# Optimization experiments

Hardware: AMD Instinct MI355X
Metric: run time of the kernel (lower is better)

Reference implementation:

```python
import jax, jax.numpy as jnp
import numpy as np

D_IN = 2048
D_OUT = 2048
NUM_HEADS = 16
HEAD_DIM = D_OUT // NUM_HEADS
LATENT = 256
B, S = 2, 2048


def setup_inputs() -> dict:
    key = jax.random.key(0)
    ks = jax.random.split(key, 7)
    s = lambda fan_in: 1.0 / np.sqrt(fan_in)
    return {
        "x": jax.random.normal(ks[0], (B, S, D_IN), dtype=jnp.float32),
        "W_query": jax.random.normal(ks[1], (D_IN, D_OUT), dtype=jnp.float32) * s(D_IN),
        "W_DKV": jax.random.normal(ks[2], (D_IN, LATENT), dtype=jnp.float32) * s(D_IN),
        "W_UK": jax.random.normal(ks[3], (LATENT, D_OUT), dtype=jnp.float32) * s(LATENT),
        "W_UV": jax.random.normal(ks[4], (LATENT, D_OUT), dtype=jnp.float32) * s(LATENT),
        "W_out": jax.random.normal(ks[5], (D_OUT, D_OUT), dtype=jnp.float32) * s(D_OUT),
        "b_out": jax.random.normal(ks[6], (D_OUT,), dtype=jnp.float32) * 0.01,
    }


def reference(x, W_query, W_DKV, W_UK, W_UV, W_out, b_out):
    b, n, _ = x.shape
    # projections
    q = x @ W_query                      # [b, n, d_out]
    latent = x @ W_DKV                   # [b, n, latent]
    k = latent @ W_UK                    # [b, n, d_out]
    v = latent @ W_UV                    # [b, n, d_out]
    # split heads -> [b, h, n, hd]
    to_heads = lambda t: t.reshape(b, n, NUM_HEADS, HEAD_DIM).transpose(0, 2, 1, 3)
    q, k, v = to_heads(q), to_heads(k), to_heads(v)
    scores = jnp.einsum("bhqd,bhkd->bhqk", q, k)
    # causal mask: q_pos < k_pos masked to -inf (applied BEFORE scaling, as in source)
    qpos = jnp.arange(n)[:, None]
    kpos = jnp.arange(n)[None, :]
    scores = jnp.where(qpos < kpos, -jnp.inf, scores)
    attn = jax.nn.softmax(scores / np.sqrt(HEAD_DIM), axis=-1)
    ctx = jnp.einsum("bhqk,bhkd->bhqd", attn, v)   # [b, h, n, hd]
    ctx = ctx.transpose(0, 2, 1, 3).reshape(b, n, D_OUT)
    return ctx @ W_out + b_out
```

## Files before the change

### kernel.cpp

```cpp
#include <hip/hip_runtime.h>

#define DIN 2048
#define DOUT 2048
#define NHEADS 16
#define HDIM 128
#define LATENT 256
#define BB 2
#define SS 2048
#define MTOT (BB*SS)
#define QLD (DOUT + LATENT)
#define KLD (2*DOUT)

using bf16 = __bf16;
using bf16x8 = __attribute__((ext_vector_type(8))) __bf16;
using f32x4 = __attribute__((ext_vector_type(4))) float;

__device__ __forceinline__ void gload16(const bf16* g, bf16* l) {
    __builtin_amdgcn_global_load_lds(
        (const __attribute__((address_space(1))) void*)g,
        (__attribute__((address_space(3))) void*)l, 16, 0, 0);
}

__global__ void cast_f32_bf16(const float* __restrict__ in, bf16* __restrict__ out, int n) {
    int i = (blockIdx.x * blockDim.x + threadIdx.x) * 8;
    if (i >= n) return;
    float4 a = *(const float4*)(in + i);
    float4 b = *(const float4*)(in + i + 4);
    bf16x8 o;
    o[0] = (bf16)a.x; o[1] = (bf16)a.y; o[2] = (bf16)a.z; o[3] = (bf16)a.w;
    o[4] = (bf16)b.x; o[5] = (bf16)b.y; o[6] = (bf16)b.z; o[7] = (bf16)b.w;
    *(bf16x8*)(out + i) = o;
}

__global__ void transpose_cast(const float* __restrict__ W, bf16* __restrict__ WT, int R, int C) {
    __shared__ float tile[32][33];
    int c0 = blockIdx.x * 32, r0 = blockIdx.y * 32;
    int tx = threadIdx.x & 31, ty = threadIdx.x >> 5;
    #pragma unroll
    for (int i = ty; i < 32; i += 8)
        tile[i][tx] = W[(size_t)(r0 + i) * C + c0 + tx];
    __syncthreads();
    #pragma unroll
    for (int i = ty; i < 32; i += 8)
        WT[(size_t)(c0 + i) * R + r0 + tx] = (bf16)tile[tx][i];
}

__global__ void transpose_v(const bf16* __restrict__ v, bf16* __restrict__ vT) {
    int bh = blockIdx.z;
    int s0 = blockIdx.x * 32, d0 = blockIdx.y * 32;
    __shared__ bf16 t[32][33];
    int tx = threadIdx.x & 31, ty = threadIdx.x >> 5;
    int b = bh >> 4, h = bh & 15;
    #pragma unroll
    for (int i = ty; i < 32; i += 8)
        t[i][tx] = v[(size_t)(b * SS + s0 + i) * KLD + h * HDIM + d0 + tx];
    __syncthreads();
    #pragma unroll
    for (int i = ty; i < 32; i += 8)
        vT[((size_t)bh * HDIM + d0 + i) * SS + s0 + tx] = t[tx][i];
}

template<bool OUT_F32, bool BIAS>
__global__ __launch_bounds__(256) void gemm_bt(const bf16* __restrict__ A,
        const bf16* __restrict__ BT, void* __restrict__ Cp,
        const float* __restrict__ bias, const int Kdim, const int Ald,
        const int Ndim, const int Cld) {
    const int nwg = gridDim.x * gridDim.y;
    int orig = blockIdx.y * gridDim.x + blockIdx.x;
    int swz = (orig & 7) * (nwg >> 3) + (orig >> 3);
    const int n0 = (swz % gridDim.x) * 128, m0 = (swz / gridDim.x) * 128;

    const int tid = threadIdx.x, wave = tid >> 6, lane = tid & 63;
    const int wm = wave >> 1, wn = wave & 1;
    const int lr = lane & 15, lg = lane >> 4;
    __shared__ __align__(16) bf16 As[128][32];
    __shared__ __align__(16) bf16 Bs[128][32];
    f32x4 acc[4][4];
    #pragma unroll
    for (int i = 0; i < 4; ++i)
        #pragma unroll
        for (int j = 0; j < 4; ++j) acc[i][j] = (f32x4){0.f, 0.f, 0.f, 0.f};

    const int sr = lane >> 2;
    const int sc = (lane & 3) * 8;
    const bf16* ga = A  + (size_t)(m0 + wave * 16 + sr) * Ald + sc;
    const bf16* gb = BT + (size_t)(n0 + wave * 16 + sr) * Kdim + sc;
    const size_t strideA64 = (size_t)64 * Ald;
    const size_t strideB64 = (size_t)64 * Kdim;
    bf16* lAd = &As[wave * 16][0];
    bf16* lBd = &Bs[wave * 16][0];

    for (int k0 = 0; k0 < Kdim; k0 += 32) {
        gload16(ga,             lAd);
        gload16(ga + strideA64, lAd + 64 * 32);
        gload16(gb,             lBd);
        gload16(gb + strideB64, lBd + 64 * 32);
        ga += 32; gb += 32;
        __syncthreads();
        bf16x8 af[4], bfr[4];
        #pragma unroll
        for (int i = 0; i < 4; ++i)
            af[i] = *(const bf16x8*)&As[wm * 64 + i * 16 + lr][lg * 8];
        #pragma unroll
        for (int j = 0; j < 4; ++j)
            bfr[j] = *(const bf16x8*)&Bs[wn * 64 + j * 16 + lr][lg * 8];
        #pragma unroll
        for (int i = 0; i < 4; ++i)
            #pragma unroll
            for (int j = 0; j < 4; ++j)
                acc[i][j] = __builtin_amdgcn_mfma_f32_16x16x32_bf16(af[i], bfr[j], acc[i][j], 0, 0, 0);
        __syncthreads();
    }
    #pragma unroll
    for (int i = 0; i < 4; ++i)
        #pragma unroll
        for (int j = 0; j < 4; ++j) {
            const int r0 = m0 + wm * 64 + i * 16 + lg * 4;
            const int c = n0 + wn * 64 + j * 16 + lr;
            #pragma unroll
            for (int r2 = 0; r2 < 4; ++r2) {
                float v = acc[i][j][r2];
                if (BIAS) v += bias[c];
                if (OUT_F32) ((float*)Cp)[(size_t)(r0 + r2) * Cld + c] = v;
                else         ((bf16*)Cp)[(size_t)(r0 + r2) * Cld + c] = (bf16)v;
            }
        }
}

__global__ __launch_bounds__(256) void attn_kernel(const bf16* __restrict__ q,
        const bf16* __restrict__ k, const bf16* __restrict__ vT, bf16* __restrict__ ctx) {
    int orig = blockIdx.y * 16 + blockIdx.x;
    int swz = (orig & 7) * 64 + (orig >> 3);
    const int bx = swz & 15, bh = swz >> 4;
    const int b = bh >> 4, h = bh & 15;
    const int tid = threadIdx.x, wave = tid >> 6, lane = tid & 63;
    const int lr = lane & 15, lg = lane >> 4;

    __shared__ __align__(16) bf16 KsL[64 * 128];
    __shared__ __align__(16) bf16 VsL[128 * 64];
    __shared__ __align__(16) bf16 PsL[64 * 64];

    char* KsB = (char*)KsL; char* VsB = (char*)VsL; char* PsB = (char*)PsL;

    const int krow = tid >> 2, kc0b = (tid & 3) * 64;
    const int vrow = tid >> 1, vc0b = (tid & 1) * 64;
    int kOff[4], vOff[4];
    #pragma unroll
    for (int u = 0; u < 4; ++u) {
        kOff[u] = (krow * 256 + kc0b + u * 16) ^ ((krow & 7) << 4);
        vOff[u] = (vrow * 128 + vc0b + u * 16) ^ ((vrow & 7) << 4);
    }
    const bf16* gkb = k  + ((size_t)b * SS + krow) * KLD + h * HDIM + (tid & 3) * 32;
    const bf16* gvb = vT + ((size_t)bh * HDIM + vrow) * SS + (tid & 1) * 32;

    const float C = 0.12751744f;

    for (int half = 0; half < 2; ++half) {
        const int qt = half ? (31 - bx) : bx;
        const int q0 = qt * 64;

        bf16x8 qf[4];
        const bf16* qbase = q + ((size_t)(b * SS + q0 + wave * 16 + lr)) * QLD + h * HDIM;
        #pragma unroll
        for (int d = 0; d < 4; ++d) qf[d] = *(const bf16x8*)(qbase + d * 32 + lg * 8);

        f32x4 o[8];
        #pragma unroll
        for (int i = 0; i < 8; ++i) o[i] = (f32x4){0.f, 0.f, 0.f, 0.f};
        float m_i[4], l_i[4];
        #pragma unroll
        for (int r = 0; r < 4; ++r) { m_i[r] = -3.0e38f; l_i[r] = 0.f; }

        const int nkt = qt + 1;
        bf16x8 kreg[4], vreg[4];
        #pragma unroll
        for (int u = 0; u < 4; ++u) {
            kreg[u] = *(const bf16x8*)(gkb + (size_t)0 * 64 * KLD + u * 8);
            vreg[u] = *(const bf16x8*)(gvb + 0 * 64 + u * 8);
        }
        #pragma unroll
        for (int u = 0; u < 4; ++u) {
            *(bf16x8*)(KsB + kOff[u]) = kreg[u];
            *(bf16x8*)(VsB + vOff[u]) = vreg[u];
        }
        __syncthreads();

        for (int kt = 0; kt < nkt; ++kt) {
            const int kbase = kt * 64;
            const bool have_next = (kt + 1 < nkt);
            if (have_next) {
                const bf16* gk = gkb + (size_t)(kt + 1) * 64 * KLD;
                const bf16* gv = gvb + (kt + 1) * 64;
                #pragma unroll
                for (int u = 0; u < 4; ++u) {
                    kreg[u] = *(const bf16x8*)(gk + u * 8);
                    vreg[u] = *(const bf16x8*)(gv + u * 8);
                }
            }

            f32x4 sacc[4];
            #pragma unroll
            for (int nf = 0; nf < 4; ++nf) sacc[nf] = (f32x4){0.f, 0.f, 0.f, 0.f};
            __builtin_amdgcn_s_setprio(1);
            #pragma unroll
            for (int nf = 0; nf < 4; ++nf)
                #pragma unroll
                for (int d = 0; d < 4; ++d) {
                    int row = nf * 16 + lr;
                    bf16x8 kf = *(const bf16x8*)(KsB + ((row * 256 + d * 64 + lg * 16) ^ ((row & 7) << 4)));
                    sacc[nf] = __builtin_amdgcn_mfma_f32_16x16x32_bf16(qf[d], kf, sacc[nf], 0, 0, 0);
                }
            __builtin_amdgcn_s_setprio(0);

            float sv[4][4];
            const bool maskt = (kbase + 63 > q0);
            #pragma unroll
            for (int nf = 0; nf < 4; ++nf)
                #pragma unroll
                for (int r = 0; r < 4; ++r) {
                    float s = sacc[nf][r];
                    if (maskt) {
                        int qr = q0 + wave * 16 + lg * 4 + r;
                        int kc = kbase + nf * 16 + lr;
                        if (qr < kc) s = -3.0e38f;
                    }
                    sv[nf][r] = s;
                }
            float corr[4];
            #pragma unroll
            for (int r = 0; r < 4; ++r) {
                float v = fmaxf(fmaxf(sv[0][r], sv[1][r]), fmaxf(sv[2][r], sv[3][r]));
                #pragma unroll
                for (int off = 1; off < 16; off <<= 1) v = fmaxf(v, __shfl_xor(v, off));
                float mnew = fmaxf(m_i[r], v);
                corr[r] = __builtin_amdgcn_exp2f((m_i[r] - mnew) * C);
                m_i[r] = mnew;
            }
            float rsum[4] = {0.f, 0.f, 0.f, 0.f};
            #pragma unroll
            for (int nf = 0; nf < 4; ++nf)
                #pragma unroll
                for (int r = 0; r < 4; ++r) {
                    float p = __builtin_amdgcn_exp2f((sv[nf][r] - m_i[r]) * C);
                    rsum[r] += p;
                    int prow = wave * 16 + lg * 4 + r;
                    *(bf16*)(PsB + ((prow * 128 + (nf * 16 + lr) * 2) ^ ((prow & 7) << 4))) = (bf16)p;
                }
            #pragma unroll
            for (int r = 0; r < 4; ++r) {
                float v = rsum[r];
                #pragma unroll
                for (int off = 1; off < 16; off <<= 1) v += __shfl_xor(v, off);
                l_i[r] = l_i[r] * corr[r] + v;
            }
            #pragma unroll
            for (int df = 0; df < 8; ++df)
                #pragma unroll
                for (int r = 0; r < 4; ++r) o[df][r] *= corr[r];

            __builtin_amdgcn_s_setprio(1);
            #pragma unroll
            for (int ks = 0; ks < 2; ++ks) {
                int prow = wave * 16 + lr;
                bf16x8 pf = *(const bf16x8*)(PsB + ((prow * 128 + ks * 64 + lg * 16) ^ ((prow & 7) << 4)));
                #pragma unroll
                for (int df = 0; df < 8; ++df) {
                    int vr2 = df * 16 + lr;
                    bf16x8 vf = *(const bf16x8*)(VsB + ((vr2 * 128 + ks * 64 + lg * 16) ^ ((vr2 & 7) << 4)));
                    o[df] = __builtin_amdgcn_mfma_f32_16x16x32_bf16(pf, vf, o[df], 0, 0, 0);
                }
            }
            __builtin_amdgcn_s_setprio(0);
            __syncthreads();
            if (have_next) {
                #pragma unroll
                for (int u = 0; u < 4; ++u) {
                    *(bf16x8*)(KsB + kOff[u]) = kreg[u];
                    *(bf16x8*)(VsB + vOff[u]) = vreg[u];
                }
            }
            __syncthreads();
        }

        #pragma unroll
        for (int r = 0; r < 4; ++r) {
            float inv = 1.0f / l_i[r];
            #pragma unroll
            for (int df = 0; df < 8; ++df) {
                int rrow = q0 + wave * 16 + lg * 4 + r;
                int col = h * HDIM + df * 16 + lr;
                ctx[(size_t)(b * SS + rrow) * DOUT + col] = (bf16)(o[df][r] * inv);
            }
        }
    }
}

extern "C" void kernel_launch(void* const* d_in, const int* in_sizes, int n_in,
                              void* d_out, int out_size, void* d_ws, size_t ws_size,
                              hipStream_t stream) {
    const float* x    = (const float*)d_in[0];
    const float* Wq   = (const float*)d_in[1];
    const float* Wdkv = (const float*)d_in[2];
    const float* Wuk  = (const float*)d_in[3];
    const float* Wuv  = (const float*)d_in[4];
    const float* Wout = (const float*)d_in[5];
    const float* bout = (const float*)d_in[6];

    char* ws = (char*)d_ws;
    size_t off = 0;
    auto alloc = [&](size_t bytes) { char* p = ws + off; off = (off + bytes + 255) & ~255ULL; return p; };
    bf16* xb    = (bf16*)alloc((size_t)MTOT * DIN * 2);
    bf16* WqT   = (bf16*)alloc((size_t)DOUT * DIN * 2);
    bf16* WdkvT = (bf16*)alloc((size_t)LATENT * DIN * 2);
    bf16* WukT  = (bf16*)alloc((size_t)DOUT * LATENT * 2);
    bf16* WuvT  = (bf16*)alloc((size_t)DOUT * LATENT * 2);
    bf16* WoutT = (bf16*)alloc((size_t)DOUT * DOUT * 2);
    bf16* qlat  = (bf16*)alloc((size_t)MTOT * QLD * 2);
    bf16* kvb   = (bf16*)alloc((size_t)MTOT * KLD * 2);
    bf16* vT    = (bf16*)alloc((size_t)BB * NHEADS * HDIM * SS * 2);
    bf16* ctx   = (bf16*)alloc((size_t)MTOT * DOUT * 2);

    cast_f32_bf16<<<(MTOT * DIN) / 8 / 256, 256, 0, stream>>>(x, xb, MTOT * DIN);
    transpose_cast<<<dim3(DOUT / 32, DIN / 32), 256, 0, stream>>>(Wq, WqT, DIN, DOUT);
    transpose_cast<<<dim3(LATENT / 32, DIN / 32), 256, 0, stream>>>(Wdkv, WdkvT, DIN, LATENT);
    transpose_cast<<<dim3(DOUT / 32, LATENT / 32), 256, 0, stream>>>(Wuk, WukT, LATENT, DOUT);
    transpose_cast<<<dim3(DOUT / 32, LATENT / 32), 256, 0, stream>>>(Wuv, WuvT, LATENT, DOUT);
    transpose_cast<<<dim3(DOUT / 32, DOUT / 32), 256, 0, stream>>>(Wout, WoutT, DOUT, DOUT);

    gemm_bt<false, false><<<dim3(QLD / 128, MTOT / 128), 256, 0, stream>>>(
        xb, WqT, qlat, nullptr, DIN, DIN, QLD, QLD);
    gemm_bt<false, false><<<dim3(KLD / 128, MTOT / 128), 256, 0, stream>>>(
        qlat + DOUT, WukT, kvb, nullptr, LATENT, QLD, KLD, KLD);

    transpose_v<<<dim3(SS / 32, HDIM / 32, BB * NHEADS), 256, 0, stream>>>(kvb + DOUT, vT);

    attn_kernel<<<dim3(16, BB * NHEADS), 256, 0, stream>>>(qlat, kvb, vT, ctx);

    gemm_bt<true, true><<<dim3(DOUT / 128, MTOT / 128), 256, 0, stream>>>(
        ctx, WoutT, d_out, bout, DOUT, DOUT, DOUT, DOUT);
}
```

Measured before the change: 444.7 us.

## Double-buffer attention K/V tiles with direct global-to-LDS async loads

Replaces the register-staged K/V prefetch in the attention kernel with global_load_lds direct-to-LDS copies into double-buffered shared tiles. This removes one of the two per-iteration barriers and the VGPRs that held the staged tiles. Launch bounds now request 4 blocks per CU. The exchange is double the K/V LDS footprint and a reliance on the async LDS writes being visible after the remaining barrier. The softmax scale constant is also nudged slightly.

```diff
diff --git a/kernel.cpp b/kernel.cpp
--- a/kernel.cpp
+++ b/kernel.cpp
@@ -127,7 +127,7 @@
         }
 }
 
-__global__ __launch_bounds__(256) void attn_kernel(const bf16* __restrict__ q,
+__global__ __launch_bounds__(256, 4) void attn_kernel(const bf16* __restrict__ q,
         const bf16* __restrict__ k, const bf16* __restrict__ vT, bf16* __restrict__ ctx) {
     int orig = blockIdx.y * 16 + blockIdx.x;
     int swz = (orig & 7) * 64 + (orig >> 3);
@@ -136,25 +136,25 @@
     const int tid = threadIdx.x, wave = tid >> 6, lane = tid & 63;
     const int lr = lane & 15, lg = lane >> 4;
 
-    __shared__ __align__(16) bf16 KsL[64 * 128];
-    __shared__ __align__(16) bf16 VsL[128 * 64];
-    __shared__ __align__(16) bf16 PsL[64 * 64];
-
-    char* KsB = (char*)KsL; char* VsB = (char*)VsL; char* PsB = (char*)PsL;
-
-    const int krow = tid >> 2, kc0b = (tid & 3) * 64;
-    const int vrow = tid >> 1, vc0b = (tid & 1) * 64;
-    int kOff[4], vOff[4];
-    #pragma unroll
-    for (int u = 0; u < 4; ++u) {
-        kOff[u] = (krow * 256 + kc0b + u * 16) ^ ((krow & 7) << 4);
-        vOff[u] = (vrow * 128 + vc0b + u * 16) ^ ((vrow & 7) << 4);
+    __shared__ __align__(16) char KsB[2 * 16384];
+    __shared__ __align__(16) char VsB[2 * 16384];
+    __shared__ __align__(16) char PsB[64 * 128];
+
+    int krow[4], kcolE[4];
+    #pragma unroll
+    for (int c = 0; c < 4; ++c) {
+        krow[c] = wave * 16 + c * 4 + (lane >> 4);
+        kcolE[c] = ((((lane & 15) * 16) ^ ((krow[c] & 7) << 4)) >> 1);
     }
-    const bf16* gkb = k  + ((size_t)b * SS + krow) * KLD + h * HDIM + (tid & 3) * 32;
-    const bf16* gvb = vT + ((size_t)bh * HDIM + vrow) * SS + (tid & 1) * 32;
-
-    const float C = 0.12751744f;
-
+    const int vrow0 = wave * 32 + (lane >> 3);
+    const int vcolE = ((((lane & 7) * 16) ^ ((lane >> 3) << 4)) >> 1);
+
+    const bf16* kbaseP = k  + (size_t)b * SS * KLD + h * HDIM;
+    const bf16* vbaseP = vT + (size_t)bh * HDIM * SS;
+
+    const float C = 0.12752602f;
+
+    int cur = 0;
     for (int half = 0; half < 2; ++half) {
         const int qt = half ? (31 - bx) : bx;
         const int q0 = qt * 64;
@@ -172,31 +172,32 @@
         for (int r = 0; r < 4; ++r) { m_i[r] = -3.0e38f; l_i[r] = 0.f; }
 
         const int nkt = qt + 1;
-        bf16x8 kreg[4], vreg[4];
-        #pragma unroll
-        for (int u = 0; u < 4; ++u) {
-            kreg[u] = *(const bf16x8*)(gkb + (size_t)0 * 64 * KLD + u * 8);
-            vreg[u] = *(const bf16x8*)(gvb + 0 * 64 + u * 8);
-        }
-        #pragma unroll
-        for (int u = 0; u < 4; ++u) {
-            *(bf16x8*)(KsB + kOff[u]) = kreg[u];
-            *(bf16x8*)(VsB + vOff[u]) = vreg[u];
+
+        {
+            bf16* dK = (bf16*)(KsB + cur * 16384 + wave * 4096);
+            bf16* dV = (bf16*)(VsB + cur * 16384 + wave * 4096);
+            #pragma unroll
+            for (int c = 0; c < 4; ++c) {
+                gload16(kbaseP + (size_t)krow[c] * KLD + kcolE[c], dK + c * 512);
+                gload16(vbaseP + (size_t)(vrow0 + c * 8) * SS + vcolE, dV + c * 512);
+            }
         }
         __syncthreads();
 
         for (int kt = 0; kt < nkt; ++kt) {
             const int kbase = kt * 64;
-            const bool have_next = (kt + 1 < nkt);
-            if (have_next) {
-                const bf16* gk = gkb + (size_t)(kt + 1) * 64 * KLD;
-                const bf16* gv = gvb + (kt + 1) * 64;
-                #pragma unroll
-                for (int u = 0; u < 4; ++u) {
-                    kreg[u] = *(const bf16x8*)(gk + u * 8);
-                    vreg[u] = *(const bf16x8*)(gv + u * 8);
-                }
-            }
+            if (kt + 1 < nkt) {
+                const int kb2 = kbase + 64;
+                bf16* dK = (bf16*)(KsB + (cur ^ 1) * 16384 + wave * 4096);
+                bf16* dV = (bf16*)(VsB + (cur ^ 1) * 16384 + wave * 4096);
+                #pragma unroll
+                for (int c = 0; c < 4; ++c) {
+                    gload16(kbaseP + (size_t)(kb2 + krow[c]) * KLD + kcolE[c], dK + c * 512);
+                    gload16(vbaseP + (size_t)(vrow0 + c * 8) * SS + kb2 + vcolE, dV + c * 512);
+                }
+            }
+            const char* KB = KsB + cur * 16384;
+            const char* VB = VsB + cur * 16384;
 
             f32x4 sacc[4];
             #pragma unroll
@@ -207,7 +208,7 @@
                 #pragma unroll
                 for (int d = 0; d < 4; ++d) {
                     int row = nf * 16 + lr;
-                    bf16x8 kf = *(const bf16x8*)(KsB + ((row * 256 + d * 64 + lg * 16) ^ ((row & 7) << 4)));
+                    bf16x8 kf = *(const bf16x8*)(KB + ((row * 256 + d * 64 + lg * 16) ^ ((row & 7) << 4)));
                     sacc[nf] = __builtin_amdgcn_mfma_f32_16x16x32_bf16(qf[d], kf, sacc[nf], 0, 0, 0);
                 }
             __builtin_amdgcn_s_setprio(0);
@@ -266,20 +267,13 @@
                 #pragma unroll
                 for (int df = 0; df < 8; ++df) {
                     int vr2 = df * 16 + lr;
-                    bf16x8 vf = *(const bf16x8*)(VsB + ((vr2 * 128 + ks * 64 + lg * 16) ^ ((vr2 & 7) << 4)));
+                    bf16x8 vf = *(const bf16x8*)(VB + ((vr2 * 128 + ks * 64 + lg * 16) ^ ((vr2 & 7) << 4)));
                     o[df] = __builtin_amdgcn_mfma_f32_16x16x32_bf16(pf, vf, o[df], 0, 0, 0);
                 }
             }
             __builtin_amdgcn_s_setprio(0);
             __syncthreads();
-            if (have_next) {
-                #pragma unroll
-                for (int u = 0; u < 4; ++u) {
-                    *(bf16x8*)(KsB + kOff[u]) = kreg[u];
-                    *(bf16x8*)(VsB + vOff[u]) = vreg[u];
-                }
-            }
-            __syncthreads();
+            cur ^= 1;
         }
 
         #pragma unroll
```

New measurement: 379.9 us. 14.6% less time.
